# Optimization experiments

Measured on AMD Instinct MI355X. Metric: run time of the kernel, lower is better.

The kernel has to match this reference:

```python
import jax, jax.numpy as jnp
import numpy as np

DT = 1e-3            # norse default integration step
TAU_MEM_INV = 50.0   # 1 / tau_mem, tau_mem = 0.02 from config
TAU_SYN_INV = 200.0  # norse default
V_TH = 1.0           # config['threshold']
ALPHA = 100.0        # SuperSpike surrogate sharpness (norse default)


@jax.custom_vjp
def spike(x):
    # Heaviside forward, SuperSpike surrogate gradient backward
    return (x > 0).astype(x.dtype)

def _spike_fwd(x):
    return (x > 0).astype(x.dtype), x

def _spike_bwd(res, g):
    return (g / (ALPHA * jnp.abs(res) + 1.0) ** 2,)

spike.defvjp(_spike_fwd, _spike_bwd)


def lif_step(v, i, inp):
    # norse lif_feed_forward_step: decay v and i, spike, reset, inject input into i
    v_dec = v + DT * TAU_MEM_INV * (-v + i)   # v_leak = 0
    i_dec = i - DT * TAU_SYN_INV * i
    s = spike(v_dec - V_TH)
    v_new = (1.0 - s) * v_dec                 # v_reset = 0
    i_new = i_dec + inp
    return s, v_new, i_new


def setup_inputs() -> dict:
    key = jax.random.key(0)
    ks = jax.random.split(key, 7)
    B, T, H, OUT = 256, 32, 1024, 10
    IN = 2 * 34 * 34  # 2312
    x = jax.random.uniform(ks[0], (B, T, 2, 34, 34), dtype=jnp.float32)
    s_in = 1.0 / np.sqrt(IN)
    s_h = 1.0 / np.sqrt(H)
    W1 = jax.random.uniform(ks[1], (H, IN), jnp.float32, -s_in, s_in)
    b1 = jax.random.uniform(ks[2], (H,), jnp.float32, -s_in, s_in)
    W2 = jax.random.uniform(ks[3], (H, H), jnp.float32, -s_h, s_h)
    b2 = jax.random.uniform(ks[4], (H,), jnp.float32, -s_h, s_h)
    Wout = jax.random.uniform(ks[5], (OUT, H), jnp.float32, -s_h, s_h)
    bout = jax.random.uniform(ks[6], (OUT,), jnp.float32, -s_h, s_h)
    return {"x": x, "W1": W1, "b1": b1, "W2": W2, "b2": b2, "Wout": Wout, "bout": bout}


def reference(x, W1, b1, W2, b2, Wout, bout):
    B, T = x.shape[0], x.shape[1]
    xt = x.reshape(B, T, -1).transpose(1, 0, 2)  # (T, B, IN): permute + flatten
    H, OUT = W1.shape[0], Wout.shape[0]
    zH = jnp.zeros((B, H), x.dtype)
    zO = jnp.zeros((B, OUT), x.dtype)
    carry0 = (zH, zH, zH, zH, zO, zO)  # (v1, i1, v2, i2, v_out, i_out)

    def step(carry, x_t):
        v1, i1, v2, i2, vo, io = carry
        s1, v1, i1 = lif_step(v1, i1, x_t @ W1.T + b1)
        s2, v2, i2 = lif_step(v2, i2, s1 @ W2.T + b2)
        so, vo, io = lif_step(vo, io, s2 @ Wout.T + bout)
        return (v1, i1, v2, i2, vo, io), so

    _, spikes = jax.lax.scan(step, carry0, xt)  # (T, B, OUT)
    return spikes.sum(axis=0)  # rate decoding -> (B, OUT)
```

## Files before the change

### kernel.cpp

```cpp
#include <hip/hip_runtime.h>


#define TB 256
#define TT 32
#define TH 1024
#define TIN 2312
#define TOUT 10
#define TM (TT * TB)
#define KP1 2368

typedef __bf16 bf16_t;
typedef bf16_t bf16x8 __attribute__((ext_vector_type(8)));
typedef bf16_t bf16x4 __attribute__((ext_vector_type(4)));
typedef _Float16 f16_t;
typedef f16_t f16x8 __attribute__((ext_vector_type(8)));
typedef f16_t f16x4 __attribute__((ext_vector_type(4)));
typedef float floatx4 __attribute__((ext_vector_type(4)));

__device__ __forceinline__ void split3(float v, bf16_t& a, bf16_t& b, bf16_t& c) {
  a = (bf16_t)v;
  float r1 = v - (float)a;
  b = (bf16_t)r1;
  c = (bf16_t)(r1 - (float)b);
}

__device__ __forceinline__ void split2h(float v, f16_t& a, f16_t& b) {
  a = (f16_t)v;
  b = (f16_t)(v - (float)a);
}

__global__ __launch_bounds__(256) void split_w(const float* __restrict__ W,
                                               bf16_t* __restrict__ P,
                                               long plane, int K, int Kp) {
  int k4 = (blockIdx.x * 256 + threadIdx.x) * 4;
  if (k4 >= Kp) return;
  long r = blockIdx.y;
  float4 v = (k4 < K) ? *(const float4*)(W + r * (long)K + k4)
                      : float4{0.f, 0.f, 0.f, 0.f};
  float t[4] = {v.x, v.y, v.z, v.w};
  bf16x4 a, b, c;
  #pragma unroll
  for (int e = 0; e < 4; ++e) {
    bf16_t x, y, z;
    split3(t[e], x, y, z);
    a[e] = x; b[e] = y; c[e] = z;
  }
  long o = r * (long)Kp + k4;
  *(bf16x4*)(P + o) = a;
  *(bf16x4*)(P + plane + o) = b;
  *(bf16x4*)(P + 2 * plane + o) = c;
}

__global__ __launch_bounds__(256) void split_w1h(const float* __restrict__ W,
                                                 f16_t* __restrict__ P,
                                                 long plane, int K, int Kp) {
  int k4 = (blockIdx.x * 256 + threadIdx.x) * 4;
  if (k4 >= Kp) return;
  long r = blockIdx.y;
  float4 v = (k4 < K) ? *(const float4*)(W + r * (long)K + k4)
                      : float4{0.f, 0.f, 0.f, 0.f};
  float t[4] = {v.x, v.y, v.z, v.w};
  f16x4 a, b;
  #pragma unroll
  for (int e = 0; e < 4; ++e) {
    f16_t x, y;
    split2h(t[e], x, y);
    a[e] = x; b[e] = y;
  }
  long o = r * (long)Kp + k4;
  *(f16x4*)(P + o) = a;
  *(f16x4*)(P + plane + o) = b;
}

__global__ __launch_bounds__(512, 4) void snn_gemm1(
    const float* __restrict__ Af, long sT, long sB,
    const f16_t* __restrict__ Bp, long planeB, int Kp, int K,
    const float* __restrict__ bias, float* __restrict__ C, int N) {
  constexpr int LDW = 36;
  __shared__ f16_t As[2][128 * LDW];
  __shared__ f16_t Bs[2][128 * LDW];

  const int tid = threadIdx.x;
  const int wave = tid >> 6, lane = tid & 63;
  const int quad = lane >> 4, l16 = lane & 15;
  const int wm = (wave & 3) * 32, wn = (wave >> 2) * 64;
  const long m0 = (long)blockIdx.x * 128, n0 = (long)blockIdx.y * 128;

  floatx4 acc[2][4];
  #pragma unroll
  for (int i = 0; i < 2; ++i)
    #pragma unroll
    for (int j = 0; j < 4; ++j) acc[i][j] = (floatx4){0.f, 0.f, 0.f, 0.f};

  const int cr = tid >> 2;
  const int cs = (tid & 3) * 8;
  float4 xv[2];
  f16x8 bv[2];

  auto prefetch = [&](int kb) {
    const long rA = m0 + cr;
    const int k0 = kb + cs;
    const float* xr = Af + (rA >> 8) * sT + (rA & 255) * sB + k0;
    xv[0] = (k0 < K) ? *(const float4*)xr : float4{0.f, 0.f, 0.f, 0.f};
    xv[1] = (k0 + 4 < K) ? *(const float4*)(xr + 4)
                         : float4{0.f, 0.f, 0.f, 0.f};
    #pragma unroll
    for (int q = 0; q < 2; ++q)
      bv[q] = *(const f16x8*)(Bp + q * planeB + (n0 + cr) * (long)Kp + k0);
  };

  auto commit = [&]() {
    const int off = cr * LDW + cs;
    f16x8 h0, h1;
    float t[8] = {xv[0].x, xv[0].y, xv[0].z, xv[0].w,
                  xv[1].x, xv[1].y, xv[1].z, xv[1].w};
    #pragma unroll
    for (int e = 0; e < 8; ++e) {
      f16_t a, b;
      split2h(t[e], a, b);
      h0[e] = a; h1[e] = b;
    }
    *(f16x8*)(&As[0][off]) = h0;
    *(f16x8*)(&As[1][off]) = h1;
    #pragma unroll
    for (int q = 0; q < 2; ++q) *(f16x8*)(&Bs[q][off]) = bv[q];
  };

  const int numT = Kp / 32;
  prefetch(0);
  for (int kt = 0; kt < numT; ++kt) {
    __syncthreads();
    commit();
    const int kbn = (kt + 1 < numT) ? (kt + 1) * 32 : 0;
    prefetch(kbn);
    __syncthreads();

    f16x8 afr[2][2];
    #pragma unroll
    for (int pa = 0; pa < 2; ++pa)
      #pragma unroll
      for (int i = 0; i < 2; ++i)
        afr[pa][i] =
            *(const f16x8*)(&As[pa][(wm + i * 16 + l16) * LDW + quad * 8]);

    #pragma unroll
    for (int pb = 0; pb < 2; ++pb) {
      f16x8 bfr[4];
      #pragma unroll
      for (int j = 0; j < 4; ++j)
        bfr[j] =
            *(const f16x8*)(&Bs[pb][(wn + j * 16 + l16) * LDW + quad * 8]);
      const int pamax = 1 - pb;
      #pragma unroll
      for (int pa = 0; pa < 2; ++pa) {
        if (pa > pamax) break;
        #pragma unroll
        for (int i = 0; i < 2; ++i)
          #pragma unroll
          for (int j = 0; j < 4; ++j)
            acc[i][j] = __builtin_amdgcn_mfma_f32_16x16x32_f16(
                afr[pa][i], bfr[j], acc[i][j], 0, 0, 0);
      }
    }
  }

  #pragma unroll
  for (int j = 0; j < 4; ++j) {
    const long col = n0 + wn + j * 16 + l16;
    const float bvv = bias[col];
    #pragma unroll
    for (int i = 0; i < 2; ++i) {
      const long row0 = m0 + wm + i * 16 + quad * 4;
      #pragma unroll
      for (int g = 0; g < 4; ++g)
        C[(row0 + g) * (long)N + col] = acc[i][j][g] + bvv;
    }
  }
}

__global__ __launch_bounds__(512, 4) void snn_gemm2(
    const bf16_t* __restrict__ Ab, long sT, long sB,
    const bf16_t* __restrict__ Bp, long planeB, int Kp,
    const float* __restrict__ bias, float* __restrict__ C, int N) {
  constexpr int LDW = 36;
  __shared__ bf16_t As[1][128 * LDW];
  __shared__ bf16_t Bs[3][128 * LDW];

  const int tid = threadIdx.x;
  const int wave = tid >> 6, lane = tid & 63;
  const int quad = lane >> 4, l16 = lane & 15;
  const int wm = (wave & 3) * 32, wn = (wave >> 2) * 64;
  const long m0 = (long)blockIdx.x * 128, n0 = (long)blockIdx.y * 128;

  floatx4 acc[2][4];
  #pragma unroll
  for (int i = 0; i < 2; ++i)
    #pragma unroll
    for (int j = 0; j < 4; ++j) acc[i][j] = (floatx4){0.f, 0.f, 0.f, 0.f};

  const int cr = tid >> 2;
  const int cs = (tid & 3) * 8;
  bf16x8 av;
  bf16x8 bv[3];

  auto prefetch = [&](int kb) {
    const long rA = m0 + cr;
    const int k0 = kb + cs;
    av = *(const bf16x8*)(Ab + (rA >> 8) * sT + (rA & 255) * sB + k0);
    #pragma unroll
    for (int q = 0; q < 3; ++q)
      bv[q] = *(const bf16x8*)(Bp + q * planeB + (n0 + cr) * (long)Kp + k0);
  };

  auto commit = [&]() {
    const int off = cr * LDW + cs;
    *(bf16x8*)(&As[0][off]) = av;
    #pragma unroll
    for (int q = 0; q < 3; ++q) *(bf16x8*)(&Bs[q][off]) = bv[q];
  };

  const int numT = Kp / 32;
  prefetch(0);
  for (int kt = 0; kt < numT; ++kt) {
    __syncthreads();
    commit();
    const int kbn = (kt + 1 < numT) ? (kt + 1) * 32 : 0;
    prefetch(kbn);
    __syncthreads();

    bf16x8 afr[2];
    #pragma unroll
    for (int i = 0; i < 2; ++i)
      afr[i] = *(const bf16x8*)(&As[0][(wm + i * 16 + l16) * LDW + quad * 8]);

    #pragma unroll
    for (int pb = 0; pb < 3; ++pb) {
      bf16x8 bfr[4];
      #pragma unroll
      for (int j = 0; j < 4; ++j)
        bfr[j] =
            *(const bf16x8*)(&Bs[pb][(wn + j * 16 + l16) * LDW + quad * 8]);
      #pragma unroll
      for (int i = 0; i < 2; ++i)
        #pragma unroll
        for (int j = 0; j < 4; ++j)
          acc[i][j] = __builtin_amdgcn_mfma_f32_16x16x32_bf16(
              afr[i], bfr[j], acc[i][j], 0, 0, 0);
    }
  }

  #pragma unroll
  for (int j = 0; j < 4; ++j) {
    const long col = n0 + wn + j * 16 + l16;
    const float bvv = bias[col];
    #pragma unroll
    for (int i = 0; i < 2; ++i) {
      const long row0 = m0 + wm + i * 16 + quad * 4;
      #pragma unroll
      for (int g = 0; g < 4; ++g)
        C[(row0 + g) * (long)N + col] = acc[i][j][g] + bvv;
    }
  }
}

__global__ __launch_bounds__(256) void lif_scan_bf16(const float* __restrict__ I,
                                                     bf16_t* __restrict__ S) {
  int idx = blockIdx.x * 256 + threadIdx.x;
  float v = 0.f, cur = 0.f;
  #pragma unroll
  for (int t = 0; t < TT; ++t) {
    float inp = I[(long)t * (TB * TH) + idx];
    float vd = fmaf(0.05f, cur - v, v);
    float id = cur - 0.2f * cur;
    float s = (vd > 1.0f) ? 1.0f : 0.f;
    v = (1.0f - s) * vd;
    cur = id + inp;
    S[(long)t * (TB * TH) + idx] = (bf16_t)s;
  }
}

__global__ __launch_bounds__(256) void gemm3_kernel(
    const bf16_t* __restrict__ S2, const float* __restrict__ Wout,
    const float* __restrict__ bout, float* __restrict__ I3) {
  int wv = (blockIdx.x * blockDim.x + threadIdx.x) >> 6;
  int lane = threadIdx.x & 63;
  if (wv >= TM) return;
  const bf16_t* srow = S2 + (long)wv * TH;
  float acc[TOUT];
  #pragma unroll
  for (int o = 0; o < TOUT; ++o) acc[o] = 0.f;
  for (int k = lane; k < TH; k += 64) {
    float s = (float)srow[k];
    #pragma unroll
    for (int o = 0; o < TOUT; ++o) acc[o] = fmaf(s, Wout[o * TH + k], acc[o]);
  }
  #pragma unroll
  for (int off = 32; off > 0; off >>= 1)
    #pragma unroll
    for (int o = 0; o < TOUT; ++o) acc[o] += __shfl_down(acc[o], off, 64);
  if (lane == 0) {
    #pragma unroll
    for (int o = 0; o < TOUT; ++o) I3[(long)wv * TOUT + o] = acc[o] + bout[o];
  }
}

__global__ __launch_bounds__(256) void scan_out(const float* __restrict__ I3,
                                                float* __restrict__ out) {
  int idx = blockIdx.x * blockDim.x + threadIdx.x;
  if (idx >= TB * TOUT) return;
  float v = 0.f, cur = 0.f, cnt = 0.f;
  #pragma unroll
  for (int t = 0; t < TT; ++t) {
    float inp = I3[(long)t * (TB * TOUT) + idx];
    float vd = fmaf(0.05f, cur - v, v);
    float id = cur - 0.2f * cur;
    float s = (vd > 1.0f) ? 1.0f : 0.f;
    v = (1.0f - s) * vd;
    cur = id + inp;
    cnt += s;
  }
  out[idx] = cnt;
}

extern "C" void kernel_launch(void* const* d_in, const int* in_sizes, int n_in,
                              void* d_out, int out_size, void* d_ws,
                              size_t ws_size, hipStream_t stream) {
  const float* x    = (const float*)d_in[0];
  const float* W1   = (const float*)d_in[1];
  const float* b1   = (const float*)d_in[2];
  const float* W2   = (const float*)d_in[3];
  const float* b2   = (const float*)d_in[4];
  const float* Wout = (const float*)d_in[5];
  const float* bout = (const float*)d_in[6];

  char* base = (char*)d_ws;
  const long S2_BYTES = (long)TM * TH * 2;
  f16_t*  W1p  = (f16_t*)base;
  bf16_t* W2p  = (bf16_t*)(base + 2L * TH * KP1 * 2);
  float*  bufI = (float*)(base + S2_BYTES);
  bf16_t* S1   = (bf16_t*)(base + S2_BYTES + (long)TM * TH * 4);
  float*  buf3 = (float*)(base + S2_BYTES + (long)TM * TH * 4 + (long)TM * TH * 2);
  bf16_t* S2   = (bf16_t*)base;

  split_w1h<<<dim3(3, TH), 256, 0, stream>>>(W1, W1p, (long)TH * KP1, TIN, KP1);
  split_w<<<dim3(1, TH), 256, 0, stream>>>(W2, W2p, (long)TH * TH, TH, TH);

  snn_gemm1<<<dim3(TM / 128, TH / 128), 512, 0, stream>>>(
      x, (long)TIN, (long)TT * TIN, W1p, (long)TH * KP1, KP1, TIN, b1, bufI,
      TH);

  lif_scan_bf16<<<(TB * TH) / 256, 256, 0, stream>>>(bufI, S1);

  snn_gemm2<<<dim3(TM / 128, TH / 128), 512, 0, stream>>>(
      S1, (long)TB * TH, (long)TH, W2p, (long)TH * TH, TH, b2, bufI, TH);

  lif_scan_bf16<<<(TB * TH) / 256, 256, 0, stream>>>(bufI, S2);

  gemm3_kernel<<<(TM * 64) / 256, 256, 0, stream>>>(S2, Wout, bout, buf3);

  scan_out<<<(TB * TOUT + 255) / 256, 256, 0, stream>>>(buf3, (float*)d_out);
}
```

Before: 334.9 us.

## Use fp16 two-plane split for W2 and enlarge GEMM tiles to 128x256

The second GEMM now splits W2 into two fp16 planes instead of three bf16 planes, and the spike activations are stored as fp16. That cuts the MFMA count and the B-operand loads for that GEMM. Both GEMMs also move from 128x128 to 128x256 block tiles, with each wave computing a 64x64 sub-tile and occupancy lowered to 2 blocks. The goal is more reuse per LDS load and fewer instructions per result. The risks are lower occupancy, higher register pressure, and slightly less accuracy in the W2 products, since two fp16 planes keep fewer mantissa bits than three bf16 planes.

```diff
diff --git a/kernel.cpp b/kernel.cpp
--- a/kernel.cpp
+++ b/kernel.cpp
@@ -9,46 +9,14 @@
 #define TM (TT * TB)
 #define KP1 2368
 
-typedef __bf16 bf16_t;
-typedef bf16_t bf16x8 __attribute__((ext_vector_type(8)));
-typedef bf16_t bf16x4 __attribute__((ext_vector_type(4)));
 typedef _Float16 f16_t;
 typedef f16_t f16x8 __attribute__((ext_vector_type(8)));
 typedef f16_t f16x4 __attribute__((ext_vector_type(4)));
 typedef float floatx4 __attribute__((ext_vector_type(4)));
 
-__device__ __forceinline__ void split3(float v, bf16_t& a, bf16_t& b, bf16_t& c) {
-  a = (bf16_t)v;
-  float r1 = v - (float)a;
-  b = (bf16_t)r1;
-  c = (bf16_t)(r1 - (float)b);
-}
-
 __device__ __forceinline__ void split2h(float v, f16_t& a, f16_t& b) {
   a = (f16_t)v;
   b = (f16_t)(v - (float)a);
-}
-
-__global__ __launch_bounds__(256) void split_w(const float* __restrict__ W,
-                                               bf16_t* __restrict__ P,
-                                               long plane, int K, int Kp) {
-  int k4 = (blockIdx.x * 256 + threadIdx.x) * 4;
-  if (k4 >= Kp) return;
-  long r = blockIdx.y;
-  float4 v = (k4 < K) ? *(const float4*)(W + r * (long)K + k4)
-                      : float4{0.f, 0.f, 0.f, 0.f};
-  float t[4] = {v.x, v.y, v.z, v.w};
-  bf16x4 a, b, c;
-  #pragma unroll
-  for (int e = 0; e < 4; ++e) {
-    bf16_t x, y, z;
-    split3(t[e], x, y, z);
-    a[e] = x; b[e] = y; c[e] = z;
-  }
-  long o = r * (long)Kp + k4;
-  *(bf16x4*)(P + o) = a;
-  *(bf16x4*)(P + plane + o) = b;
-  *(bf16x4*)(P + 2 * plane + o) = c;
 }
 
 __global__ __launch_bounds__(256) void split_w1h(const float* __restrict__ W,
@@ -72,30 +40,32 @@
   *(f16x4*)(P + plane + o) = b;
 }
 
-__global__ __launch_bounds__(512, 4) void snn_gemm1(
+__global__ __launch_bounds__(512, 2) void snn_gemm1(
     const float* __restrict__ Af, long sT, long sB,
     const f16_t* __restrict__ Bp, long planeB, int Kp, int K,
     const float* __restrict__ bias, float* __restrict__ C, int N) {
   constexpr int LDW = 36;
   __shared__ f16_t As[2][128 * LDW];
-  __shared__ f16_t Bs[2][128 * LDW];
+  __shared__ f16_t Bs[2][256 * LDW];
 
   const int tid = threadIdx.x;
   const int wave = tid >> 6, lane = tid & 63;
   const int quad = lane >> 4, l16 = lane & 15;
-  const int wm = (wave & 3) * 32, wn = (wave >> 2) * 64;
-  const long m0 = (long)blockIdx.x * 128, n0 = (long)blockIdx.y * 128;
-
-  floatx4 acc[2][4];
-  #pragma unroll
-  for (int i = 0; i < 2; ++i)
+  const int wm = (wave & 1) * 64, wn = (wave >> 1) * 64;
+  const long m0 = (long)blockIdx.x * 128, n0 = (long)blockIdx.y * 256;
+
+  floatx4 acc[4][4];
+  #pragma unroll
+  for (int i = 0; i < 4; ++i)
     #pragma unroll
     for (int j = 0; j < 4; ++j) acc[i][j] = (floatx4){0.f, 0.f, 0.f, 0.f};
 
   const int cr = tid >> 2;
   const int cs = (tid & 3) * 8;
+  const int crB = tid >> 1;
+  const int csB = (tid & 1) * 16;
   float4 xv[2];
-  f16x8 bv[2];
+  f16x8 bv[2][2];
 
   auto prefetch = [&](int kb) {
     const long rA = m0 + cr;
@@ -104,9 +74,13 @@
     xv[0] = (k0 < K) ? *(const float4*)xr : float4{0.f, 0.f, 0.f, 0.f};
     xv[1] = (k0 + 4 < K) ? *(const float4*)(xr + 4)
                          : float4{0.f, 0.f, 0.f, 0.f};
-    #pragma unroll
-    for (int q = 0; q < 2; ++q)
-      bv[q] = *(const f16x8*)(Bp + q * planeB + (n0 + cr) * (long)Kp + k0);
+    const int kB = kb + csB;
+    #pragma unroll
+    for (int q = 0; q < 2; ++q) {
+      const f16_t* br = Bp + q * planeB + (n0 + crB) * (long)Kp + kB;
+      bv[q][0] = *(const f16x8*)br;
+      bv[q][1] = *(const f16x8*)(br + 8);
+    }
   };
 
   auto commit = [&]() {
@@ -122,8 +96,12 @@
     }
     *(f16x8*)(&As[0][off]) = h0;
     *(f16x8*)(&As[1][off]) = h1;
-    #pragma unroll
-    for (int q = 0; q < 2; ++q) *(f16x8*)(&Bs[q][off]) = bv[q];
+    const int offB = crB * LDW + csB;
+    #pragma unroll
+    for (int q = 0; q < 2; ++q) {
+      *(f16x8*)(&Bs[q][offB]) = bv[q][0];
+      *(f16x8*)(&Bs[q][offB + 8]) = bv[q][1];
+    }
   };
 
   const int numT = Kp / 32;
@@ -135,11 +113,11 @@
     prefetch(kbn);
     __syncthreads();
 
-    f16x8 afr[2][2];
+    f16x8 afr[2][4];
     #pragma unroll
     for (int pa = 0; pa < 2; ++pa)
       #pragma unroll
-      for (int i = 0; i < 2; ++i)
+      for (int i = 0; i < 4; ++i)
         afr[pa][i] =
             *(const f16x8*)(&As[pa][(wm + i * 16 + l16) * LDW + quad * 8]);
 
@@ -155,7 +133,7 @@
       for (int pa = 0; pa < 2; ++pa) {
         if (pa > pamax) break;
         #pragma unroll
-        for (int i = 0; i < 2; ++i)
+        for (int i = 0; i < 4; ++i)
           #pragma unroll
           for (int j = 0; j < 4; ++j)
             acc[i][j] = __builtin_amdgcn_mfma_f32_16x16x32_f16(
@@ -169,7 +147,7 @@
     const long col = n0 + wn + j * 16 + l16;
     const float bvv = bias[col];
     #pragma unroll
-    for (int i = 0; i < 2; ++i) {
+    for (int i = 0; i < 4; ++i) {
       const long row0 = m0 + wm + i * 16 + quad * 4;
       #pragma unroll
       for (int g = 0; g < 4; ++g)
@@ -178,45 +156,53 @@
   }
 }
 
-__global__ __launch_bounds__(512, 4) void snn_gemm2(
-    const bf16_t* __restrict__ Ab, long sT, long sB,
-    const bf16_t* __restrict__ Bp, long planeB, int Kp,
+__global__ __launch_bounds__(512, 2) void snn_gemm2(
+    const f16_t* __restrict__ Ab, long sT, long sB,
+    const f16_t* __restrict__ Bp, long planeB, int Kp,
     const float* __restrict__ bias, float* __restrict__ C, int N) {
   constexpr int LDW = 36;
-  __shared__ bf16_t As[1][128 * LDW];
-  __shared__ bf16_t Bs[3][128 * LDW];
+  __shared__ f16_t As[128 * LDW];
+  __shared__ f16_t Bs[2][256 * LDW];
 
   const int tid = threadIdx.x;
   const int wave = tid >> 6, lane = tid & 63;
   const int quad = lane >> 4, l16 = lane & 15;
-  const int wm = (wave & 3) * 32, wn = (wave >> 2) * 64;
-  const long m0 = (long)blockIdx.x * 128, n0 = (long)blockIdx.y * 128;
-
-  floatx4 acc[2][4];
-  #pragma unroll
-  for (int i = 0; i < 2; ++i)
+  const int wm = (wave & 1) * 64, wn = (wave >> 1) * 64;
+  const long m0 = (long)blockIdx.x * 128, n0 = (long)blockIdx.y * 256;
+
+  floatx4 acc[4][4];
+  #pragma unroll
+  for (int i = 0; i < 4; ++i)
     #pragma unroll
     for (int j = 0; j < 4; ++j) acc[i][j] = (floatx4){0.f, 0.f, 0.f, 0.f};
 
   const int cr = tid >> 2;
   const int cs = (tid & 3) * 8;
-  bf16x8 av;
-  bf16x8 bv[3];
+  const int crB = tid >> 1;
+  const int csB = (tid & 1) * 16;
+  f16x8 av;
+  f16x8 bv[2][2];
 
   auto prefetch = [&](int kb) {
     const long rA = m0 + cr;
-    const int k0 = kb + cs;
-    av = *(const bf16x8*)(Ab + (rA >> 8) * sT + (rA & 255) * sB + k0);
-    #pragma unroll
-    for (int q = 0; q < 3; ++q)
-      bv[q] = *(const bf16x8*)(Bp + q * planeB + (n0 + cr) * (long)Kp + k0);
+    av = *(const f16x8*)(Ab + (rA >> 8) * sT + (rA & 255) * sB + kb + cs);
+    const int kB = kb + csB;
+    #pragma unroll
+    for (int q = 0; q < 2; ++q) {
+      const f16_t* br = Bp + q * planeB + (n0 + crB) * (long)Kp + kB;
+      bv[q][0] = *(const f16x8*)br;
+      bv[q][1] = *(const f16x8*)(br + 8);
+    }
   };
 
   auto commit = [&]() {
-    const int off = cr * LDW + cs;
-    *(bf16x8*)(&As[0][off]) = av;
-    #pragma unroll
-    for (int q = 0; q < 3; ++q) *(bf16x8*)(&Bs[q][off]) = bv[q];
+    *(f16x8*)(&As[cr * LDW + cs]) = av;
+    const int offB = crB * LDW + csB;
+    #pragma unroll
+    for (int q = 0; q < 2; ++q) {
+      *(f16x8*)(&Bs[q][offB]) = bv[q][0];
+      *(f16x8*)(&Bs[q][offB + 8]) = bv[q][1];
+    }
   };
 
   const int numT = Kp / 32;
@@ -228,23 +214,23 @@
     prefetch(kbn);
     __syncthreads();
 
-    bf16x8 afr[2];
-    #pragma unroll
-    for (int i = 0; i < 2; ++i)
-      afr[i] = *(const bf16x8*)(&As[0][(wm + i * 16 + l16) * LDW + quad * 8]);
-
-    #pragma unroll
-    for (int pb = 0; pb < 3; ++pb) {
-      bf16x8 bfr[4];
+    f16x8 afr[4];
+    #pragma unroll
+    for (int i = 0; i < 4; ++i)
+      afr[i] = *(const f16x8*)(&As[(wm + i * 16 + l16) * LDW + quad * 8]);
+
+    #pragma unroll
+    for (int pb = 0; pb < 2; ++pb) {
+      f16x8 bfr[4];
       #pragma unroll
       for (int j = 0; j < 4; ++j)
         bfr[j] =
-            *(const bf16x8*)(&Bs[pb][(wn + j * 16 + l16) * LDW + quad * 8]);
-      #pragma unroll
-      for (int i = 0; i < 2; ++i)
+            *(const f16x8*)(&Bs[pb][(wn + j * 16 + l16) * LDW + quad * 8]);
+      #pragma unroll
+      for (int i = 0; i < 4; ++i)
         #pragma unroll
         for (int j = 0; j < 4; ++j)
-          acc[i][j] = __builtin_amdgcn_mfma_f32_16x16x32_bf16(
+          acc[i][j] = __builtin_amdgcn_mfma_f32_16x16x32_f16(
               afr[i], bfr[j], acc[i][j], 0, 0, 0);
     }
   }
@@ -254,7 +240,7 @@
     const long col = n0 + wn + j * 16 + l16;
     const float bvv = bias[col];
     #pragma unroll
-    for (int i = 0; i < 2; ++i) {
+    for (int i = 0; i < 4; ++i) {
       const long row0 = m0 + wm + i * 16 + quad * 4;
       #pragma unroll
       for (int g = 0; g < 4; ++g)
@@ -263,8 +249,8 @@
   }
 }
 
-__global__ __launch_bounds__(256) void lif_scan_bf16(const float* __restrict__ I,
-                                                     bf16_t* __restrict__ S) {
+__global__ __launch_bounds__(256) void lif_scan_f16(const float* __restrict__ I,
+                                                    f16_t* __restrict__ S) {
   int idx = blockIdx.x * 256 + threadIdx.x;
   float v = 0.f, cur = 0.f;
   #pragma unroll
@@ -275,17 +261,17 @@
     float s = (vd > 1.0f) ? 1.0f : 0.f;
     v = (1.0f - s) * vd;
     cur = id + inp;
-    S[(long)t * (TB * TH) + idx] = (bf16_t)s;
+    S[(long)t * (TB * TH) + idx] = (f16_t)s;
   }
 }
 
 __global__ __launch_bounds__(256) void gemm3_kernel(
-    const bf16_t* __restrict__ S2, const float* __restrict__ Wout,
+    const f16_t* __restrict__ S2, const float* __restrict__ Wout,
     const float* __restrict__ bout, float* __restrict__ I3) {
   int wv = (blockIdx.x * blockDim.x + threadIdx.x) >> 6;
   int lane = threadIdx.x & 63;
   if (wv >= TM) return;
-  const bf16_t* srow = S2 + (long)wv * TH;
+  const f16_t* srow = S2 + (long)wv * TH;
   float acc[TOUT];
   #pragma unroll
   for (int o = 0; o < TOUT; ++o) acc[o] = 0.f;
@@ -335,26 +321,26 @@
 
   char* base = (char*)d_ws;
   const long S2_BYTES = (long)TM * TH * 2;
-  f16_t*  W1p  = (f16_t*)base;
-  bf16_t* W2p  = (bf16_t*)(base + 2L * TH * KP1 * 2);
-  float*  bufI = (float*)(base + S2_BYTES);
-  bf16_t* S1   = (bf16_t*)(base + S2_BYTES + (long)TM * TH * 4);
-  float*  buf3 = (float*)(base + S2_BYTES + (long)TM * TH * 4 + (long)TM * TH * 2);
-  bf16_t* S2   = (bf16_t*)base;
+  f16_t* W1p  = (f16_t*)base;
+  f16_t* W2p  = (f16_t*)(base + 2L * TH * KP1 * 2);
+  float* bufI = (float*)(base + S2_BYTES);
+  f16_t* S1   = (f16_t*)(base + S2_BYTES + (long)TM * TH * 4);
+  float* buf3 = (float*)(base + S2_BYTES + (long)TM * TH * 4 + (long)TM * TH * 2);
+  f16_t* S2   = (f16_t*)base;
 
   split_w1h<<<dim3(3, TH), 256, 0, stream>>>(W1, W1p, (long)TH * KP1, TIN, KP1);
-  split_w<<<dim3(1, TH), 256, 0, stream>>>(W2, W2p, (long)TH * TH, TH, TH);
-
-  snn_gemm1<<<dim3(TM / 128, TH / 128), 512, 0, stream>>>(
+  split_w1h<<<dim3(1, TH), 256, 0, stream>>>(W2, W2p, (long)TH * TH, TH, TH);
+
+  snn_gemm1<<<dim3(TM / 128, TH / 256), 512, 0, stream>>>(
       x, (long)TIN, (long)TT * TIN, W1p, (long)TH * KP1, KP1, TIN, b1, bufI,
       TH);
 
-  lif_scan_bf16<<<(TB * TH) / 256, 256, 0, stream>>>(bufI, S1);
-
-  snn_gemm2<<<dim3(TM / 128, TH / 128), 512, 0, stream>>>(
+  lif_scan_f16<<<(TB * TH) / 256, 256, 0, stream>>>(bufI, S1);
+
+  snn_gemm2<<<dim3(TM / 128, TH / 256), 512, 0, stream>>>(
       S1, (long)TB * TH, (long)TH, W2p, (long)TH * TH, TH, b2, bufI, TH);
 
-  lif_scan_bf16<<<(TB * TH) / 256, 256, 0, stream>>>(bufI, S2);
+  lif_scan_f16<<<(TB * TH) / 256, 256, 0, stream>>>(bufI, S2);
 
   gemm3_kernel<<<(TM * 64) / 256, 256, 0, stream>>>(S2, Wout, bout, buf3);
 
```

After: 332.0 us. Within noise of the previous version (-0.9%).
